# Kernel tuning notes

Hardware: AMD Instinct MI355X
Metric: run time of the kernel (lower is better)

The kernel has to match this reference:

```python
import jax, jax.numpy as jnp
import numpy as np
import math

EPS = 1e-06
C_CONST = 2.0 + EPS
CHUNK = 128


def _features(xc, omega, W_poly, quad_nodes):
    # xc: (B,H,t,D) -> poly:(B,H,t,P), prf:(R,B,H,t,M)
    xn = xc / jnp.clip(jnp.linalg.norm(xc, axis=-1, keepdims=True), 1e-12)  # F.normalize
    poly = jnp.einsum('bhtd,hdp->bhtp', xn, W_poly)
    proj = jnp.einsum('bhtd,rhdm->rbhtm', xn, omega)
    s = quad_nodes[:, None, None, None, None]
    sqrt2s = jnp.sqrt(2.0 * jnp.clip(s, 0.0))
    M = omega.shape[-1]
    prf = jnp.exp(jnp.clip(proj * sqrt2s - s, -20.0, 20.0)) / math.sqrt(M)
    return poly, prf


def setup_inputs() -> dict:
    key = jax.random.key(0)
    ks = jax.random.split(key, 6)
    B, T, E, H, D, M, R, P = 1, 1024, 512, 8, 64, 8, 1, 32
    x = jax.random.normal(ks[0], (B, T, E), jnp.float32)
    W_qkv = jax.random.normal(ks[1], (3 * E, E), jnp.float32) / math.sqrt(E)
    b_qkv = jnp.zeros((3 * E,), jnp.float32)
    W_out = jax.random.normal(ks[2], (E, E), jnp.float32) / math.sqrt(E)
    b_out = jnp.zeros((E,), jnp.float32)
    omega = jax.random.normal(ks[3], (R, H, D, M), jnp.float32)
    W_poly = jax.random.normal(ks[4], (H, D, P), jnp.float32) / math.sqrt(D)
    nodes, weights = np.polynomial.laguerre.laggauss(R)
    quad_nodes = jnp.asarray(nodes, jnp.float32) / C_CONST
    quad_weights = jnp.asarray(weights, jnp.float32) / C_CONST
    return {"x": x, "W_qkv": W_qkv, "b_qkv": b_qkv, "W_out": W_out, "b_out": b_out,
            "omega": omega, "W_poly": W_poly, "quad_nodes": quad_nodes, "quad_weights": quad_weights}


def reference(x, W_qkv, b_qkv, W_out, b_out, omega, W_poly, quad_nodes, quad_weights):
    B, T, E = x.shape
    R, H, D, M = omega.shape
    P = W_poly.shape[-1]
    qkv = x @ W_qkv.T + b_qkv
    q, k, v = jnp.split(qkv, 3, axis=-1)

    def to_chunks(a):
        # (B,T,E) -> (Nc,B,H,chunk,D)
        return a.reshape(B, T, H, D).transpose(0, 2, 1, 3).reshape(B, H, T // CHUNK, CHUNK, D).transpose(2, 0, 1, 3, 4)

    qc, kc, vc = map(to_chunks, (q, k, v))
    sqw = jnp.sqrt(jnp.clip(quad_weights, 0.0))[:, None, None, None, None]
    kv0 = jnp.zeros((R, B, H, P, M, D), jnp.float32)
    k0 = jnp.zeros((R, B, H, P, M), jnp.float32)

    def step(carry, inp):
        kv_state, k_state = carry
        qch, kch, vch = inp
        q_poly, q_prf = _features(qch, omega, W_poly, quad_nodes)
        k_poly, k_prf = _features(kch, omega, W_poly, quad_nodes)
        q_prf = q_prf * sqw
        k_prf = k_prf * sqw
        q_outer = jnp.einsum('bhtp,rbhtm->rbhtpm', q_poly, q_prf)
        k_outer = jnp.einsum('bhtp,rbhtm->rbhtpm', k_poly, k_prf)
        kv_prod = jnp.einsum('rbhtpm,bhtd->rbhtpmd', k_outer, vch)
        kv_cur = jnp.cumsum(kv_prod, axis=3) + kv_state[:, :, :, None]
        k_cur = jnp.cumsum(k_outer, axis=3) + k_state[:, :, :, None]
        ctx = jnp.einsum('rbhtpm,rbhtpmd->bhtd', q_outer, kv_cur)  # sums over r too
        den = jnp.einsum('rbhtpm,rbhtpm->bht', q_outer, k_cur)
        out = ctx / jnp.clip(den, 1e-06)[..., None]
        return (kv_cur[:, :, :, -1], k_cur[:, :, :, -1]), out

    _, outs = jax.lax.scan(step, (kv0, k0), (qc, kc, vc))  # (Nc,B,H,chunk,D)
    out = outs.transpose(1, 2, 0, 3, 4).reshape(B, H, T, D).transpose(0, 2, 1, 3).reshape(B, T, E)
    return out @ W_out.T + b_out
```

## Files before the change

### kernel.cpp

```cpp
#include <hip/hip_runtime.h>
#include <math.h>


__global__ __launch_bounds__(256) void gemm_bias_kernel(
    const float* __restrict__ A, const float* __restrict__ W,
    const float* __restrict__ bias, float* __restrict__ C,
    int M, int N, int K)
{
    __shared__ float a_t[16][68];
    __shared__ float w_t[16][68];
    const int tid = threadIdx.x;
    const int n0 = blockIdx.x * 64;
    const int m0 = blockIdx.y * 64;
    const int tx = tid & 15, ty = tid >> 4;
    const int lrow = tid >> 2;
    const int lk4  = (tid & 3) * 4;
    float acc[4][4];
#pragma unroll
    for (int i = 0; i < 4; ++i)
#pragma unroll
        for (int j = 0; j < 4; ++j) acc[i][j] = 0.f;

    const float* Ap = &A[(m0 + lrow) * K + lk4];
    const float* Wp = &W[(n0 + lrow) * K + lk4];
    float4 ra = *(const float4*)Ap;
    float4 rw = *(const float4*)Wp;

    for (int k0 = 0; k0 < K; k0 += 16) {
        a_t[lk4 + 0][lrow] = ra.x; a_t[lk4 + 1][lrow] = ra.y;
        a_t[lk4 + 2][lrow] = ra.z; a_t[lk4 + 3][lrow] = ra.w;
        w_t[lk4 + 0][lrow] = rw.x; w_t[lk4 + 1][lrow] = rw.y;
        w_t[lk4 + 2][lrow] = rw.z; w_t[lk4 + 3][lrow] = rw.w;
        __syncthreads();
        if (k0 + 16 < K) {
            ra = *(const float4*)(Ap + k0 + 16);
            rw = *(const float4*)(Wp + k0 + 16);
        }
#pragma unroll
        for (int k = 0; k < 16; ++k) {
            float4 af = *(const float4*)&a_t[k][ty * 4];
            float4 wf = *(const float4*)&w_t[k][tx * 4];
            acc[0][0] += af.x * wf.x; acc[0][1] += af.x * wf.y;
            acc[0][2] += af.x * wf.z; acc[0][3] += af.x * wf.w;
            acc[1][0] += af.y * wf.x; acc[1][1] += af.y * wf.y;
            acc[1][2] += af.y * wf.z; acc[1][3] += af.y * wf.w;
            acc[2][0] += af.z * wf.x; acc[2][1] += af.z * wf.y;
            acc[2][2] += af.z * wf.z; acc[2][3] += af.z * wf.w;
            acc[3][0] += af.w * wf.x; acc[3][1] += af.w * wf.y;
            acc[3][2] += af.w * wf.z; acc[3][3] += af.w * wf.w;
        }
        __syncthreads();
    }
    float4 bv = *(const float4*)&bias[n0 + tx * 4];
#pragma unroll
    for (int i = 0; i < 4; ++i) {
        float4 o;
        o.x = acc[i][0] + bv.x; o.y = acc[i][1] + bv.y;
        o.z = acc[i][2] + bv.z; o.w = acc[i][3] + bv.w;
        *(float4*)&C[(m0 + ty * 4 + i) * N + n0 + tx * 4] = o;
    }
}

__global__ __launch_bounds__(256) void features_kernel(
    const float* __restrict__ qkv, const float* __restrict__ omega,
    const float* __restrict__ W_poly, const float* __restrict__ qn,
    const float* __restrict__ qw, float* __restrict__ phi_q,
    float* __restrict__ phi_k)
{
    __shared__ float xn[4][2][64];
    __shared__ float poly[4][2][32];
    __shared__ float prf[4][2][8];
    const int tid = threadIdx.x;
    const int w = tid >> 6;
    const int lane = tid & 63;
    const int item = blockIdx.x * 4 + w;
    const int h = item >> 10;
    const int t = item & 1023;

    float xq = qkv[t * 1536 + h * 64 + lane];
    float xk = qkv[t * 1536 + 512 + h * 64 + lane];
    float sq = xq * xq, sk = xk * xk;
#pragma unroll
    for (int o = 32; o; o >>= 1) { sq += __shfl_xor(sq, o); sk += __shfl_xor(sk, o); }
    float xnq = xq / fmaxf(sqrtf(sq), 1e-12f);
    float xnk = xk / fmaxf(sqrtf(sk), 1e-12f);
    xn[w][0][lane] = xnq;
    xn[w][1][lane] = xnk;
    __syncthreads();

    {
        const int which = lane >> 5;
        const int p = lane & 31;
        float pacc = 0.f;
#pragma unroll 8
        for (int d = 0; d < 64; ++d)
            pacc += xn[w][which][d] * W_poly[(h * 64 + d) * 32 + p];
        poly[w][which][p] = pacc;
    }
    if (lane < 16) {
        const int wh2 = lane >> 3, m = lane & 7;
        float pr = 0.f;
#pragma unroll 8
        for (int d = 0; d < 64; ++d)
            pr += xn[w][wh2][d] * omega[(h * 64 + d) * 8 + m];
        float s0 = qn[0];
        float sqrt2s = sqrtf(2.f * fmaxf(s0, 0.f));
        float sqw = sqrtf(fmaxf(qw[0], 0.f));
        float z = fminf(fmaxf(pr * sqrt2s - s0, -20.f), 20.f);
        prf[w][wh2][m] = expf(z) * 0.3535533905932738f * sqw;
    }
    __syncthreads();

    const int pp = lane >> 1;
    const int mb = (lane & 1) * 4;
    float qp = poly[w][0][pp], kp = poly[w][1][pp];
    float4 oq, ok;
    oq.x = qp * prf[w][0][mb + 0]; oq.y = qp * prf[w][0][mb + 1];
    oq.z = qp * prf[w][0][mb + 2]; oq.w = qp * prf[w][0][mb + 3];
    ok.x = kp * prf[w][1][mb + 0]; ok.y = kp * prf[w][1][mb + 1];
    ok.z = kp * prf[w][1][mb + 2]; ok.w = kp * prf[w][1][mb + 3];
    *(float4*)&phi_q[((h << 10) + t) * 256 + lane * 4] = oq;
    *(float4*)&phi_k[((h << 10) + t) * 256 + lane * 4] = ok;
}

__global__ __launch_bounds__(256) void chunksum_kernel(
    const float* __restrict__ phi_k, const float* __restrict__ qkv,
    float* __restrict__ S_chunk, float* __restrict__ z_chunk)
{
    __shared__ float pk[128][64];
    __shared__ float vv[128][64];
    const int tid = threadIdx.x;
    const int h  = blockIdx.x >> 5;
    const int c  = (blockIdx.x >> 2) & 7;
    const int fg = blockIdx.x & 3;
    const int f0 = fg * 64;

#pragma unroll
    for (int i = 0; i < 8; ++i) {
        int e4 = i * 256 + tid;
        int s = e4 >> 4;
        int f4 = (e4 & 15) * 4;
        *(float4*)&pk[s][f4] =
            *(const float4*)&phi_k[((h << 10) + c * 128 + s) * 256 + f0 + f4];
    }
#pragma unroll
    for (int i = 0; i < 8; ++i) {
        int e4 = i * 256 + tid;
        int s = e4 >> 4;
        int d4 = (e4 & 15) * 4;
        *(float4*)&vv[s][d4] =
            *(const float4*)&qkv[(c * 128 + s) * 1536 + 1024 + h * 64 + d4];
    }
    __syncthreads();

    const int tx = tid & 15;
    const int ty = tid >> 4;
    float acc[4][4];
#pragma unroll
    for (int i = 0; i < 4; ++i)
#pragma unroll
        for (int j = 0; j < 4; ++j) acc[i][j] = 0.f;

    for (int s = 0; s < 128; ++s) {
        float4 pv = *(const float4*)&pk[s][ty * 4];
        float4 v4 = *(const float4*)&vv[s][tx * 4];
        acc[0][0] += pv.x * v4.x; acc[0][1] += pv.x * v4.y;
        acc[0][2] += pv.x * v4.z; acc[0][3] += pv.x * v4.w;
        acc[1][0] += pv.y * v4.x; acc[1][1] += pv.y * v4.y;
        acc[1][2] += pv.y * v4.z; acc[1][3] += pv.y * v4.w;
        acc[2][0] += pv.z * v4.x; acc[2][1] += pv.z * v4.y;
        acc[2][2] += pv.z * v4.z; acc[2][3] += pv.z * v4.w;
        acc[3][0] += pv.w * v4.x; acc[3][1] += pv.w * v4.y;
        acc[3][2] += pv.w * v4.z; acc[3][3] += pv.w * v4.w;
    }

    if (tid < 64) {
        float zacc = 0.f;
        for (int s = 0; s < 128; ++s) zacc += pk[s][tid];
        z_chunk[(h * 8 + c) * 256 + f0 + tid] = zacc;
    }

#pragma unroll
    for (int i = 0; i < 4; ++i) {
        float4 o = make_float4(acc[i][0], acc[i][1], acc[i][2], acc[i][3]);
        *(float4*)&S_chunk[((h * 8 + c) * 256 + f0 + ty * 4 + i) * 64 + tx * 4] = o;
    }
}

__global__ __launch_bounds__(256) void scan_kernel(
    const float* __restrict__ S_chunk, const float* __restrict__ z_chunk,
    float* __restrict__ S_prev, float* __restrict__ z_prev)
{
    int gid = blockIdx.x * 256 + threadIdx.x;
    if (gid < 8 * 256 * 64) {
        int h = gid >> 14;
        int r = gid & 16383;
        float acc = 0.f;
#pragma unroll
        for (int c = 0; c < 8; ++c) {
            int idx = ((h * 8 + c) << 14) + r;
            S_prev[idx] = acc;
            acc += S_chunk[idx];
        }
    }
    if (gid < 2048) {
        int h = gid >> 8, f = gid & 255;
        float acc = 0.f;
#pragma unroll
        for (int c = 0; c < 8; ++c) {
            int idx = (h * 8 + c) * 256 + f;
            z_prev[idx] = acc;
            acc += z_chunk[idx];
        }
    }
}

__global__ __launch_bounds__(512, 1) void attn_kernel(
    const float* __restrict__ phi_q, const float* __restrict__ phi_k,
    const float* __restrict__ qkv, const float* __restrict__ S_prev,
    const float* __restrict__ z_prev, float* __restrict__ attn)
{
    __shared__ float v_lds[128 * 64];
    __shared__ float A_lds[32 * 132];
    __shared__ float phq_t[32][36];
    __shared__ float phk_t[32][132];
    __shared__ float Sst[32][68];
    __shared__ float ctx_lds[32][64];
    __shared__ float z_lds[256];
    __shared__ float den_lds[32];
    const int tid = threadIdx.x;
    const int h = blockIdx.x >> 3, c = blockIdx.x & 7;
    const int tb = blockIdx.y * 32;
    const int SMAX = tb + 32;

    const int hc128 = (h << 10) + c * 128;
    const int hcS   = (h * 8 + c) * 256;

    for (int e4 = tid; e4 < SMAX * 16; e4 += 512) {
        int s = e4 >> 4;
        int d4 = (e4 & 15) * 4;
        *(float4*)&v_lds[s * 64 + d4] =
            *(const float4*)&qkv[(c * 128 + s) * 1536 + 1024 + h * 64 + d4];
    }
    if (tid < 256) z_lds[tid] = z_prev[hcS + tid];

    const int fidx = tid & 31;
    const int srow = tid >> 5;
    const int frow = tid >> 6;
    const int sdd  = tid & 63;

    const int tt = tid >> 5, ss = tid & 31;
    const bool ssActive = (ss * 4) < SMAX;
    const int u = tid & 255;
    const int d = u & 63, tg = u >> 6;

    float acc[4][4];
    float acc2[8];
    float den_acc = 0.f;
#pragma unroll
    for (int i = 0; i < 4; ++i)
#pragma unroll
        for (int j = 0; j < 4; ++j) acc[i][j] = 0.f;
#pragma unroll
    for (int i = 0; i < 8; ++i) acc2[i] = 0.f;

    float r_q0, r_q1, r_k[8], r_s[4];
#define LOAD_SLICE(F0)                                                        \
    do {                                                                      \
        r_q0 = phi_q[((hc128 + tb + srow) << 8) + (F0) + fidx];               \
        r_q1 = phi_q[((hc128 + tb + srow + 16) << 8) + (F0) + fidx];          \
        _Pragma("unroll")                                                     \
        for (int k = 0; k < 8; ++k) {                                         \
            int s_ = srow + 16 * k;                                           \
            r_k[k] = (s_ < SMAX) ? phi_k[((hc128 + s_) << 8) + (F0) + fidx]   \
                                 : 0.f;                                       \
        }                                                                     \
        _Pragma("unroll")                                                     \
        for (int k = 0; k < 4; ++k)                                           \
            r_s[k] = S_prev[((hcS + (F0) + frow + 8 * k) << 6) + sdd];        \
    } while (0)

    LOAD_SLICE(0);

    for (int ft = 0; ft < 8; ++ft) {
        const int f0 = ft * 32;
        __syncthreads();
        phq_t[fidx][srow]      = r_q0;
        phq_t[fidx][srow + 16] = r_q1;
#pragma unroll
        for (int k = 0; k < 8; ++k) phk_t[fidx][srow + 16 * k] = r_k[k];
#pragma unroll
        for (int k = 0; k < 4; ++k) Sst[frow + 8 * k][sdd] = r_s[k];
        __syncthreads();
        if (ft < 7) LOAD_SLICE(f0 + 32);

        if (tid < 256) {
            if (ssActive) {
#pragma unroll 4
                for (int f = 0; f < 32; ++f) {
                    float4 av = *(const float4*)&phq_t[f][tt * 4];
                    float4 bv = *(const float4*)&phk_t[f][ss * 4];
                    acc[0][0] += av.x * bv.x; acc[0][1] += av.x * bv.y;
                    acc[0][2] += av.x * bv.z; acc[0][3] += av.x * bv.w;
                    acc[1][0] += av.y * bv.x; acc[1][1] += av.y * bv.y;
                    acc[1][2] += av.y * bv.z; acc[1][3] += av.y * bv.w;
                    acc[2][0] += av.z * bv.x; acc[2][1] += av.z * bv.y;
                    acc[2][2] += av.z * bv.z; acc[2][3] += av.z * bv.w;
                    acc[3][0] += av.w * bv.x; acc[3][1] += av.w * bv.y;
                    acc[3][2] += av.w * bv.z; acc[3][3] += av.w * bv.w;
                }
            }
        } else {
#pragma unroll 4
            for (int f = 0; f < 32; ++f) {
                float sval = Sst[f][d];
                float4 a0 = *(const float4*)&phq_t[f][tg * 8];
                float4 a1 = *(const float4*)&phq_t[f][tg * 8 + 4];
                acc2[0] += a0.x * sval; acc2[1] += a0.y * sval;
                acc2[2] += a0.z * sval; acc2[3] += a0.w * sval;
                acc2[4] += a1.x * sval; acc2[5] += a1.y * sval;
                acc2[6] += a1.z * sval; acc2[7] += a1.w * sval;
            }
            if (u < 32) {
#pragma unroll
                for (int f = 0; f < 32; ++f)
                    den_acc += phq_t[f][u] * z_lds[f0 + f];
            }
        }
    }
#undef LOAD_SLICE

    if (tid < 256) {
        if (ssActive) {
#pragma unroll
            for (int i = 0; i < 4; ++i) {
                float4 o = make_float4(acc[i][0], acc[i][1], acc[i][2], acc[i][3]);
                *(float4*)&A_lds[(tt * 4 + i) * 132 + ss * 4] = o;
            }
        }
    } else {
#pragma unroll
        for (int i = 0; i < 8; ++i)
            ctx_lds[tg * 8 + i][d] = acc2[i];
        if (u < 32) den_lds[u] = den_acc;
    }
    __syncthreads();

    const int dd = tid & 63;
    const int rg = tid >> 6;
#pragma unroll
    for (int i = 0; i < 4; ++i) {
        int tl = rg * 4 + i;
        int tcr = tb + tl;
        float ctx = ctx_lds[tl][dd];
        float den = den_lds[tl];
        for (int s = 0; s <= tcr; ++s) {
            float a = A_lds[tl * 132 + s];
            ctx += a * v_lds[s * 64 + dd];
            den += a;
        }
        attn[(c * 128 + tcr) * 512 + h * 64 + dd] = ctx / fmaxf(den, 1e-6f);
    }
}

extern "C" void kernel_launch(void* const* d_in, const int* in_sizes, int n_in,
                              void* d_out, int out_size, void* d_ws, size_t ws_size,
                              hipStream_t stream)
{
    const float* x      = (const float*)d_in[0];
    const float* W_qkv  = (const float*)d_in[1];
    const float* b_qkv  = (const float*)d_in[2];
    const float* W_out  = (const float*)d_in[3];
    const float* b_out  = (const float*)d_in[4];
    const float* omega  = (const float*)d_in[5];
    const float* W_poly = (const float*)d_in[6];
    const float* qn     = (const float*)d_in[7];
    const float* qw     = (const float*)d_in[8];
    float* out = (float*)d_out;

    float* ws    = (float*)d_ws;
    float* qkv   = ws;
    float* phi_q = qkv + 1572864;
    float* phi_k = phi_q + 2097152;
    float* S_c   = phi_k + 2097152;
    float* z_c   = S_c + 1048576;
    float* S_p   = z_c + 16384;
    float* z_p   = S_p + 1048576;
    float* attn  = z_p + 16384;

    gemm_bias_kernel<<<dim3(24, 16), 256, 0, stream>>>(x, W_qkv, b_qkv, qkv, 1024, 1536, 512);
    features_kernel<<<2048, 256, 0, stream>>>(qkv, omega, W_poly, qn, qw, phi_q, phi_k);
    chunksum_kernel<<<256, 256, 0, stream>>>(phi_k, qkv, S_c, z_c);
    scan_kernel<<<512, 256, 0, stream>>>(S_c, z_c, S_p, z_p);
    attn_kernel<<<dim3(64, 4), 512, 0, stream>>>(phi_q, phi_k, qkv, S_p, z_p, attn);
    gemm_bias_kernel<<<dim3(8, 16), 256, 0, stream>>>(attn, W_out, b_out, out, 1024, 512, 512);
}
```

Baseline: 182.0 us.

## Split-K both GEMMs with double-buffered LDS and a separate bias reduction

Both projection GEMMs become split-K: the QKV GEMM is split into 2 K-slices and the output GEMM into 4. Each slice writes partial sums, and a new reduce kernel adds the slices plus the bias. The goal is more workgroups on the GPU (the output GEMM previously launched only 128 blocks). The tile loop also double-buffers its shared memory so it needs one barrier per step instead of two. The cost is extra partial-sum memory traffic and two extra kernel launches.

```diff
diff --git a/kernel.cpp b/kernel.cpp
--- a/kernel.cpp
+++ b/kernel.cpp
@@ -2,16 +2,17 @@
 #include <math.h>
 
 
-__global__ __launch_bounds__(256) void gemm_bias_kernel(
+__global__ __launch_bounds__(256) void gemm_part_kernel(
     const float* __restrict__ A, const float* __restrict__ W,
-    const float* __restrict__ bias, float* __restrict__ C,
-    int M, int N, int K)
-{
-    __shared__ float a_t[16][68];
-    __shared__ float w_t[16][68];
+    float* __restrict__ part, int M, int N, int K, int Kc)
+{
+    __shared__ float a_t[2][16][68];
+    __shared__ float w_t[2][16][68];
     const int tid = threadIdx.x;
     const int n0 = blockIdx.x * 64;
     const int m0 = blockIdx.y * 64;
+    const int sk = blockIdx.z;
+    const int kb = sk * Kc;
     const int tx = tid & 15, ty = tid >> 4;
     const int lrow = tid >> 2;
     const int lk4  = (tid & 3) * 4;
@@ -21,25 +22,27 @@
 #pragma unroll
         for (int j = 0; j < 4; ++j) acc[i][j] = 0.f;
 
-    const float* Ap = &A[(m0 + lrow) * K + lk4];
-    const float* Wp = &W[(n0 + lrow) * K + lk4];
+    const float* Ap = &A[(m0 + lrow) * K + kb + lk4];
+    const float* Wp = &W[(n0 + lrow) * K + kb + lk4];
     float4 ra = *(const float4*)Ap;
     float4 rw = *(const float4*)Wp;
-
-    for (int k0 = 0; k0 < K; k0 += 16) {
-        a_t[lk4 + 0][lrow] = ra.x; a_t[lk4 + 1][lrow] = ra.y;
-        a_t[lk4 + 2][lrow] = ra.z; a_t[lk4 + 3][lrow] = ra.w;
-        w_t[lk4 + 0][lrow] = rw.x; w_t[lk4 + 1][lrow] = rw.y;
-        w_t[lk4 + 2][lrow] = rw.z; w_t[lk4 + 3][lrow] = rw.w;
-        __syncthreads();
-        if (k0 + 16 < K) {
-            ra = *(const float4*)(Ap + k0 + 16);
-            rw = *(const float4*)(Wp + k0 + 16);
+    a_t[0][lk4 + 0][lrow] = ra.x; a_t[0][lk4 + 1][lrow] = ra.y;
+    a_t[0][lk4 + 2][lrow] = ra.z; a_t[0][lk4 + 3][lrow] = ra.w;
+    w_t[0][lk4 + 0][lrow] = rw.x; w_t[0][lk4 + 1][lrow] = rw.y;
+    w_t[0][lk4 + 2][lrow] = rw.z; w_t[0][lk4 + 3][lrow] = rw.w;
+    __syncthreads();
+
+    int cur = 0;
+    for (int k0 = 16; k0 <= Kc; k0 += 16) {
+        const bool more = (k0 < Kc);
+        if (more) {
+            ra = *(const float4*)(Ap + k0);
+            rw = *(const float4*)(Wp + k0);
         }
 #pragma unroll
         for (int k = 0; k < 16; ++k) {
-            float4 af = *(const float4*)&a_t[k][ty * 4];
-            float4 wf = *(const float4*)&w_t[k][tx * 4];
+            float4 af = *(const float4*)&a_t[cur][k][ty * 4];
+            float4 wf = *(const float4*)&w_t[cur][k][tx * 4];
             acc[0][0] += af.x * wf.x; acc[0][1] += af.x * wf.y;
             acc[0][2] += af.x * wf.z; acc[0][3] += af.x * wf.w;
             acc[1][0] += af.y * wf.x; acc[1][1] += af.y * wf.y;
@@ -49,16 +52,37 @@
             acc[3][0] += af.w * wf.x; acc[3][1] += af.w * wf.y;
             acc[3][2] += af.w * wf.z; acc[3][3] += af.w * wf.w;
         }
-        __syncthreads();
-    }
-    float4 bv = *(const float4*)&bias[n0 + tx * 4];
+        if (more) {
+            const int nxt = cur ^ 1;
+            a_t[nxt][lk4 + 0][lrow] = ra.x; a_t[nxt][lk4 + 1][lrow] = ra.y;
+            a_t[nxt][lk4 + 2][lrow] = ra.z; a_t[nxt][lk4 + 3][lrow] = ra.w;
+            w_t[nxt][lk4 + 0][lrow] = rw.x; w_t[nxt][lk4 + 1][lrow] = rw.y;
+            w_t[nxt][lk4 + 2][lrow] = rw.z; w_t[nxt][lk4 + 3][lrow] = rw.w;
+            __syncthreads();
+            cur = nxt;
+        }
+    }
 #pragma unroll
     for (int i = 0; i < 4; ++i) {
-        float4 o;
-        o.x = acc[i][0] + bv.x; o.y = acc[i][1] + bv.y;
-        o.z = acc[i][2] + bv.z; o.w = acc[i][3] + bv.w;
-        *(float4*)&C[(m0 + ty * 4 + i) * N + n0 + tx * 4] = o;
-    }
+        float4 o = make_float4(acc[i][0], acc[i][1], acc[i][2], acc[i][3]);
+        *(float4*)&part[((size_t)sk * M + m0 + ty * 4 + i) * N + n0 + tx * 4] = o;
+    }
+}
+
+__global__ __launch_bounds__(256) void reduce_bias_kernel(
+    const float* __restrict__ part, const float* __restrict__ bias,
+    float* __restrict__ C, int MN, int N, int S)
+{
+    const int i4 = (blockIdx.x * 256 + threadIdx.x) * 4;
+    if (i4 >= MN) return;
+    float4 acc = *(const float4*)&part[i4];
+    for (int s = 1; s < S; ++s) {
+        float4 p = *(const float4*)&part[(size_t)s * MN + i4];
+        acc.x += p.x; acc.y += p.y; acc.z += p.z; acc.w += p.w;
+    }
+    float4 b = *(const float4*)&bias[i4 % N];
+    acc.x += b.x; acc.y += b.y; acc.z += b.z; acc.w += b.w;
+    *(float4*)&C[i4] = acc;
 }
 
 __global__ __launch_bounds__(256) void features_kernel(
@@ -378,20 +402,24 @@
     const float* qw     = (const float*)d_in[8];
     float* out = (float*)d_out;
 
-    float* ws    = (float*)d_ws;
-    float* qkv   = ws;
-    float* phi_q = qkv + 1572864;
-    float* phi_k = phi_q + 2097152;
-    float* S_c   = phi_k + 2097152;
-    float* z_c   = S_c + 1048576;
-    float* S_p   = z_c + 16384;
-    float* z_p   = S_p + 1048576;
-    float* attn  = z_p + 16384;
-
-    gemm_bias_kernel<<<dim3(24, 16), 256, 0, stream>>>(x, W_qkv, b_qkv, qkv, 1024, 1536, 512);
+    float* ws     = (float*)d_ws;
+    float* qkv    = ws;
+    float* phi_q  = qkv + 1572864;
+    float* phi_k  = phi_q + 2097152;
+    float* S_c    = phi_k + 2097152;
+    float* z_c    = S_c + 1048576;
+    float* S_p    = z_c + 16384;
+    float* z_p    = S_p + 1048576;
+    float* attn   = z_p + 16384;
+    float* p_qkv  = attn + 524288;
+    float* p_out  = p_qkv + 3145728;
+
+    gemm_part_kernel<<<dim3(24, 16, 2), 256, 0, stream>>>(x, W_qkv, p_qkv, 1024, 1536, 512, 256);
+    reduce_bias_kernel<<<1536, 256, 0, stream>>>(p_qkv, b_qkv, qkv, 1572864, 1536, 2);
     features_kernel<<<2048, 256, 0, stream>>>(qkv, omega, W_poly, qn, qw, phi_q, phi_k);
     chunksum_kernel<<<256, 256, 0, stream>>>(phi_k, qkv, S_c, z_c);
     scan_kernel<<<512, 256, 0, stream>>>(S_c, z_c, S_p, z_p);
     attn_kernel<<<dim3(64, 4), 512, 0, stream>>>(phi_q, phi_k, qkv, S_p, z_p, attn);
-    gemm_bias_kernel<<<dim3(8, 16), 256, 0, stream>>>(attn, W_out, b_out, out, 1024, 512, 512);
-}
+    gemm_part_kernel<<<dim3(8, 16, 4), 256, 0, stream>>>(attn, W_out, p_out, 1024, 512, 512, 128);
+    reduce_bias_kernel<<<512, 256, 0, stream>>>(p_out, b_out, out, 524288, 512, 4);
+}
```

After: 168.9 us. 1.08x faster.
